# Performance work log

Measured on AMD Instinct MI355X. Metric: run time of the kernel, lower is better.

The kernel has to match this reference:

```python
import jax, jax.numpy as jnp
import numpy as np

NUM_EXPERTS = 8
HIDDEN = 1024
INTER = 2816
T = 16          # tokens
TOP_K = 2       # active experts per token
INIT_STD = 0.02


def setup_inputs() -> dict:
    key = jax.random.key(0)
    k_x, k_idx, k_g, k_u, k_d = jax.random.split(key, 5)
    x = jax.random.normal(k_x, (T, HIDDEN), dtype=jnp.float32)
    expert_indices = jax.random.randint(k_idx, (T, TOP_K), 0, NUM_EXPERTS)
    gate_proj = INIT_STD * jax.random.normal(k_g, (NUM_EXPERTS, INTER, HIDDEN), dtype=jnp.float32)
    up_proj = INIT_STD * jax.random.normal(k_u, (NUM_EXPERTS, HIDDEN, INTER), dtype=jnp.float32)
    down_proj = INIT_STD * jax.random.normal(k_d, (NUM_EXPERTS, INTER, HIDDEN), dtype=jnp.float32)
    return {"x": x, "expert_indices": expert_indices,
            "gate_proj": gate_proj, "up_proj": up_proj, "down_proj": down_proj}


def reference(x, expert_indices, gate_proj, up_proj, down_proj):
    # Faithful to the torch module, including its swapped proj naming:
    #   gate branch: gate_proj[idx] : [t, a, I, H]
    #   'down' branch (acts as up): down_proj[idx] : [t, a, I, H]
    #   final contraction: up_proj[idx] : [t, a, H, I]
    gw = gate_proj[expert_indices]          # [t, a, I, H]
    dw = down_proj[expert_indices]          # [t, a, I, H]
    uw = up_proj[expert_indices]            # [t, a, H, I]
    x1 = jax.nn.silu(jnp.einsum('ti,taoi->tao', x, gw))  # [t, a, I]
    x3 = jnp.einsum('ti,taoi->tao', x, dw)               # [t, a, I]
    expert_outs = jnp.einsum('tao,taio->tai', x1 * x3, uw)  # [t, a, H]
    return expert_outs
```

## Files before the change

### kernel.cpp

```cpp
#include <hip/hip_runtime.h>

#define NE 8
#define HD 1024
#define IW 2816
#define NT 16
#define TK 2
#define NP (NT*TK)

__device__ __forceinline__ float wave_sum(float v) {
    #pragma unroll
    for (int off = 32; off > 0; off >>= 1) v += __shfl_xor(v, off, 64);
    return v;
}

__global__ __launch_bounds__(256) void moe_phase1(
    const float* __restrict__ x,
    const int*   __restrict__ idx,
    const float* __restrict__ gate,
    const float* __restrict__ down,
    float*       __restrict__ hbuf)
{
    __shared__ int s_list[NP];
    __shared__ int s_n;
    const int e = blockIdx.y;
    if (threadIdx.x == 0) {
        int n = 0;
        for (int p = 0; p < NP; ++p) if (idx[p] == e) s_list[n++] = p;
        s_n = n;
    }
    __syncthreads();
    const int npl = s_n;
    if (npl == 0) return;

    const int wave = threadIdx.x >> 6;
    const int lane = threadIdx.x & 63;
    const int o = blockIdx.x * 4 + wave;
    if (o >= IW) return;

    const float* grow = gate + ((size_t)e * IW + o) * HD;
    const float* drow = down + ((size_t)e * IW + o) * HD;
    float gw[16], dw[16];
    #pragma unroll
    for (int c = 0; c < 4; ++c) {
        float4 gv = *(const float4*)(grow + c * 256 + lane * 4);
        float4 dv = *(const float4*)(drow + c * 256 + lane * 4);
        gw[4*c+0]=gv.x; gw[4*c+1]=gv.y; gw[4*c+2]=gv.z; gw[4*c+3]=gv.w;
        dw[4*c+0]=dv.x; dw[4*c+1]=dv.y; dw[4*c+2]=dv.z; dw[4*c+3]=dv.w;
    }

    for (int n = 0; n < npl; ++n) {
        const int p = s_list[n];
        const float* xrow = x + (size_t)(p >> 1) * HD;
        float ag = 0.f, ad = 0.f;
        #pragma unroll
        for (int c = 0; c < 4; ++c) {
            float4 xv = *(const float4*)(xrow + c * 256 + lane * 4);
            ag += xv.x*gw[4*c+0] + xv.y*gw[4*c+1] + xv.z*gw[4*c+2] + xv.w*gw[4*c+3];
            ad += xv.x*dw[4*c+0] + xv.y*dw[4*c+1] + xv.z*dw[4*c+2] + xv.w*dw[4*c+3];
        }
        ag = wave_sum(ag);
        ad = wave_sum(ad);
        if (lane == 0) {
            float s = ag / (1.f + __expf(-ag));
            hbuf[(size_t)p * IW + o] = s * ad;
        }
    }
}

__global__ __launch_bounds__(256) void moe_phase2(
    const float* __restrict__ up,
    const int*   __restrict__ idx,
    const float* __restrict__ hbuf,
    float*       __restrict__ out)
{
    __shared__ int s_list[NP];
    __shared__ int s_n;
    const int e = blockIdx.y;
    if (threadIdx.x == 0) {
        int n = 0;
        for (int p = 0; p < NP; ++p) if (idx[p] == e) s_list[n++] = p;
        s_n = n;
    }
    __syncthreads();
    const int npl = s_n;
    if (npl == 0) return;

    const int wave = threadIdx.x >> 6;
    const int lane = threadIdx.x & 63;
    const int h = blockIdx.x * 4 + wave;
    if (h >= HD) return;

    const float* urow = up + ((size_t)e * HD + h) * IW;
    float w[44];
    #pragma unroll
    for (int c = 0; c < 11; ++c) {
        float4 uv = *(const float4*)(urow + c * 256 + lane * 4);
        w[4*c+0]=uv.x; w[4*c+1]=uv.y; w[4*c+2]=uv.z; w[4*c+3]=uv.w;
    }

    for (int n = 0; n < npl; ++n) {
        const int p = s_list[n];
        const float* hrow = hbuf + (size_t)p * IW;
        float acc = 0.f;
        #pragma unroll
        for (int c = 0; c < 11; ++c) {
            float4 hv = *(const float4*)(hrow + c * 256 + lane * 4);
            acc += w[4*c+0]*hv.x + w[4*c+1]*hv.y + w[4*c+2]*hv.z + w[4*c+3]*hv.w;
        }
        acc = wave_sum(acc);
        if (lane == 0) out[(size_t)p * HD + h] = acc;
    }
}

extern "C" void kernel_launch(void* const* d_in, const int* in_sizes, int n_in,
                              void* d_out, int out_size, void* d_ws, size_t ws_size,
                              hipStream_t stream) {
    const float* x    = (const float*)d_in[0];
    const int*   idx  = (const int*)  d_in[1];
    const float* gate = (const float*)d_in[2];
    const float* up   = (const float*)d_in[3];
    const float* down = (const float*)d_in[4];
    float* hbuf = (float*)d_ws;
    float* out  = (float*)d_out;

    moe_phase1<<<dim3(IW/4, NE), dim3(256), 0, stream>>>(x, idx, gate, down, hbuf);
    moe_phase2<<<dim3(HD/4, NE), dim3(256), 0, stream>>>(up, idx, hbuf, out);
}
```

Baseline: 279.9 us.

## Stage token activations in LDS and stream multiple weight rows per wave

```diff
diff --git a/kernel.cpp b/kernel.cpp
--- a/kernel.cpp
+++ b/kernel.cpp
@@ -6,12 +6,34 @@
 #define NT 16
 #define TK 2
 #define NP (NT*TK)
+#define NPC1 8
+#define ROWS1 8
+#define NPC2 4
+#define ROWS2 2
 
-__device__ __forceinline__ float wave_sum(float v) {
-    #pragma unroll
-    for (int off = 32; off > 0; off >>= 1) v += __shfl_xor(v, off, 64);
-    return v;
-}
+#define LOADW(G, D, r) { _Pragma("unroll") \
+    for (int c = 0; c < 4; ++c) { \
+        float4 gv = *(const float4*)(gp + (size_t)(r) * HD + c * 256); \
+        float4 dv = *(const float4*)(dp + (size_t)(r) * HD + c * 256); \
+        G[4*c+0]=gv.x; G[4*c+1]=gv.y; G[4*c+2]=gv.z; G[4*c+3]=gv.w; \
+        D[4*c+0]=dv.x; D[4*c+1]=dv.y; D[4*c+2]=dv.z; D[4*c+3]=dv.w; } }
+
+#define COMPROW(G, D, r) { \
+    float ag[NPC1], ad[NPC1]; \
+    _Pragma("unroll") for (int j = 0; j < NPC1; ++j) { ag[j]=0.f; ad[j]=0.f; } \
+    _Pragma("unroll") for (int j = 0; j < NPC1; ++j) if (j < nc) { \
+        _Pragma("unroll") for (int c = 0; c < 4; ++c) { \
+            float4 xv = *(const float4*)&s_x[j][c*256 + lane*4]; \
+            ag[j] += xv.x*G[4*c+0] + xv.y*G[4*c+1] + xv.z*G[4*c+2] + xv.w*G[4*c+3]; \
+            ad[j] += xv.x*D[4*c+0] + xv.y*D[4*c+1] + xv.z*D[4*c+2] + xv.w*D[4*c+3]; } } \
+    _Pragma("unroll") for (int off = 32; off > 0; off >>= 1) { \
+        _Pragma("unroll") for (int j = 0; j < NPC1; ++j) if (j < nc) { \
+            ag[j] += __shfl_xor(ag[j], off, 64); \
+            ad[j] += __shfl_xor(ad[j], off, 64); } } \
+    if (lane == 0) { _Pragma("unroll") for (int j = 0; j < NPC1; ++j) if (j < nc) { \
+        const float g = ag[j]; \
+        const float s = g / (1.f + __expf(-g)); \
+        hbuf[(size_t)s_list[g0 + j] * IW + (o0 + (r))] = s * ad[j]; } } }
 
 __global__ __launch_bounds__(256) void moe_phase1(
     const float* __restrict__ x,
@@ -20,13 +42,16 @@
     const float* __restrict__ down,
     float*       __restrict__ hbuf)
 {
+    __shared__ float s_x[NPC1][HD];
     __shared__ int s_list[NP];
     __shared__ int s_n;
     const int e = blockIdx.y;
-    if (threadIdx.x == 0) {
-        int n = 0;
-        for (int p = 0; p < NP; ++p) if (idx[p] == e) s_list[n++] = p;
-        s_n = n;
+    {
+        const int t = threadIdx.x;
+        const bool mine = (t < NP) && (idx[t] == e);
+        const unsigned long long m = __ballot(mine);
+        if (mine) s_list[__popcll(m & ((1ull << t) - 1ull))] = t;
+        if (t == 0) s_n = (int)__popcll(m);
     }
     __syncthreads();
     const int npl = s_n;
@@ -34,38 +59,59 @@
 
     const int wave = threadIdx.x >> 6;
     const int lane = threadIdx.x & 63;
-    const int o = blockIdx.x * 4 + wave;
-    if (o >= IW) return;
+    const int o0 = (blockIdx.x * 4 + wave) * ROWS1;
+    const float* gp = gate + ((size_t)e * IW + o0) * HD + lane * 4;
+    const float* dp = down + ((size_t)e * IW + o0) * HD + lane * 4;
 
-    const float* grow = gate + ((size_t)e * IW + o) * HD;
-    const float* drow = down + ((size_t)e * IW + o) * HD;
-    float gw[16], dw[16];
-    #pragma unroll
-    for (int c = 0; c < 4; ++c) {
-        float4 gv = *(const float4*)(grow + c * 256 + lane * 4);
-        float4 dv = *(const float4*)(drow + c * 256 + lane * 4);
-        gw[4*c+0]=gv.x; gw[4*c+1]=gv.y; gw[4*c+2]=gv.z; gw[4*c+3]=gv.w;
-        dw[4*c+0]=dv.x; dw[4*c+1]=dv.y; dw[4*c+2]=dv.z; dw[4*c+3]=dv.w;
-    }
+    for (int g0 = 0; g0 < npl; g0 += NPC1) {
+        const int nc = (npl - g0 < NPC1) ? (npl - g0) : NPC1;
+        __syncthreads();
+        {
+            const int t = threadIdx.x;
+            for (int j = 0; j < nc; ++j) {
+                const int tok = s_list[g0 + j] >> 1;
+                *(float4*)&s_x[j][t * 4] = *(const float4*)(x + (size_t)tok * HD + t * 4);
+            }
+        }
+        __syncthreads();
 
-    for (int n = 0; n < npl; ++n) {
-        const int p = s_list[n];
-        const float* xrow = x + (size_t)(p >> 1) * HD;
-        float ag = 0.f, ad = 0.f;
-        #pragma unroll
-        for (int c = 0; c < 4; ++c) {
-            float4 xv = *(const float4*)(xrow + c * 256 + lane * 4);
-            ag += xv.x*gw[4*c+0] + xv.y*gw[4*c+1] + xv.z*gw[4*c+2] + xv.w*gw[4*c+3];
-            ad += xv.x*dw[4*c+0] + xv.y*dw[4*c+1] + xv.z*dw[4*c+2] + xv.w*dw[4*c+3];
-        }
-        ag = wave_sum(ag);
-        ad = wave_sum(ad);
-        if (lane == 0) {
-            float s = ag / (1.f + __expf(-ag));
-            hbuf[(size_t)p * IW + o] = s * ad;
-        }
+        float gA[16], dA[16], gB[16], dB[16];
+        LOADW(gA, dA, 0);
+        LOADW(gB, dB, 1);
+        COMPROW(gA, dA, 0);
+        LOADW(gA, dA, 2);
+        COMPROW(gB, dB, 1);
+        LOADW(gB, dB, 3);
+        COMPROW(gA, dA, 2);
+        LOADW(gA, dA, 4);
+        COMPROW(gB, dB, 3);
+        LOADW(gB, dB, 5);
+        COMPROW(gA, dA, 4);
+        LOADW(gA, dA, 6);
+        COMPROW(gB, dB, 5);
+        LOADW(gB, dB, 7);
+        COMPROW(gA, dA, 6);
+        COMPROW(gB, dB, 7);
     }
 }
+
+#define LOADU(W, r) { _Pragma("unroll") \
+    for (int c = 0; c < 11; ++c) { \
+        float4 uv = *(const float4*)(upp + (size_t)(r) * IW + c * 256); \
+        W[4*c+0]=uv.x; W[4*c+1]=uv.y; W[4*c+2]=uv.z; W[4*c+3]=uv.w; } }
+
+#define COMPH(W, r) { \
+    float acc[NPC2]; \
+    _Pragma("unroll") for (int j = 0; j < NPC2; ++j) acc[j] = 0.f; \
+    _Pragma("unroll") for (int j = 0; j < NPC2; ++j) if (j < nc) { \
+        _Pragma("unroll") for (int c = 0; c < 11; ++c) { \
+            float4 hv = *(const float4*)&s_h[j][c*256 + lane*4]; \
+            acc[j] += W[4*c+0]*hv.x + W[4*c+1]*hv.y + W[4*c+2]*hv.z + W[4*c+3]*hv.w; } } \
+    _Pragma("unroll") for (int off = 32; off > 0; off >>= 1) { \
+        _Pragma("unroll") for (int j = 0; j < NPC2; ++j) if (j < nc) \
+            acc[j] += __shfl_xor(acc[j], off, 64); } \
+    if (lane == 0) { _Pragma("unroll") for (int j = 0; j < NPC2; ++j) if (j < nc) \
+        out[(size_t)s_list[g0 + j] * HD + (h0 + (r))] = acc[j]; } }
 
 __global__ __launch_bounds__(256) void moe_phase2(
     const float* __restrict__ up,
@@ -73,13 +119,16 @@
     const float* __restrict__ hbuf,
     float*       __restrict__ out)
 {
+    __shared__ float s_h[NPC2][IW];
     __shared__ int s_list[NP];
     __shared__ int s_n;
     const int e = blockIdx.y;
-    if (threadIdx.x == 0) {
-        int n = 0;
-        for (int p = 0; p < NP; ++p) if (idx[p] == e) s_list[n++] = p;
-        s_n = n;
+    {
+        const int t = threadIdx.x;
+        const bool mine = (t < NP) && (idx[t] == e);
+        const unsigned long long m = __ballot(mine);
+        if (mine) s_list[__popcll(m & ((1ull << t) - 1ull))] = t;
+        if (t == 0) s_n = (int)__popcll(m);
     }
     __syncthreads();
     const int npl = s_n;
@@ -87,28 +136,27 @@
 
     const int wave = threadIdx.x >> 6;
     const int lane = threadIdx.x & 63;
-    const int h = blockIdx.x * 4 + wave;
-    if (h >= HD) return;
+    const int h0 = (blockIdx.x * 4 + wave) * ROWS2;
+    const float* upp = up + ((size_t)e * HD + h0) * IW + lane * 4;
 
-    const float* urow = up + ((size_t)e * HD + h) * IW;
-    float w[44];
-    #pragma unroll
-    for (int c = 0; c < 11; ++c) {
-        float4 uv = *(const float4*)(urow + c * 256 + lane * 4);
-        w[4*c+0]=uv.x; w[4*c+1]=uv.y; w[4*c+2]=uv.z; w[4*c+3]=uv.w;
-    }
+    for (int g0 = 0; g0 < npl; g0 += NPC2) {
+        const int nc = (npl - g0 < NPC2) ? (npl - g0) : NPC2;
+        __syncthreads();
+        {
+            const int t = threadIdx.x;
+            for (int j = 0; j < nc; ++j) {
+                const float* hr = hbuf + (size_t)s_list[g0 + j] * IW;
+                for (int k = t; k < IW / 4; k += 256)
+                    *(float4*)&s_h[j][k * 4] = *(const float4*)(hr + k * 4);
+            }
+        }
+        __syncthreads();
 
-    for (int n = 0; n < npl; ++n) {
-        const int p = s_list[n];
-        const float* hrow = hbuf + (size_t)p * IW;
-        float acc = 0.f;
-        #pragma unroll
-        for (int c = 0; c < 11; ++c) {
-            float4 hv = *(const float4*)(hrow + c * 256 + lane * 4);
-            acc += w[4*c+0]*hv.x + w[4*c+1]*hv.y + w[4*c+2]*hv.z + w[4*c+3]*hv.w;
-        }
-        acc = wave_sum(acc);
-        if (lane == 0) out[(size_t)p * HD + h] = acc;
+        float wA[44], wB[44];
+        LOADU(wA, 0);
+        LOADU(wB, 1);
+        COMPH(wA, 0);
+        COMPH(wB, 1);
     }
 }
 
@@ -123,6 +171,6 @@
     float* hbuf = (float*)d_ws;
     float* out  = (float*)d_out;
 
-    moe_phase1<<<dim3(IW/4, NE), dim3(256), 0, stream>>>(x, idx, gate, down, hbuf);
-    moe_phase2<<<dim3(HD/4, NE), dim3(256), 0, stream>>>(up, idx, hbuf, out);
+    moe_phase1<<<dim3(IW / (4 * ROWS1), NE), dim3(256), 0, stream>>>(x, idx, gate, down, hbuf);
+    moe_phase2<<<dim3(HD / (4 * ROWS2), NE), dim3(256), 0, stream>>>(up, idx, hbuf, out);
 }
```

Measured after the change: 342.5 us. +22.3%, slower.
